# Kernel tuning notes

Hardware: AMD Instinct MI355X
Metric: run time of the kernel (lower is better)

Reference implementation:

```python
import jax, jax.numpy as jnp
import numpy as np

B, S, H, N_IN, N_OUT = 8, 2048, 16, 128, 128


def setup_inputs() -> dict:
    key = jax.random.key(0)
    k1, k2 = jax.random.split(key)
    inputs = jax.random.normal(k1, (B, S, H, N_IN), dtype=jnp.float32)
    # stacked ParameterList: W[h] is the (n_out, n_in) block for head h
    W = jax.random.normal(k2, (H, N_OUT, N_IN), dtype=jnp.float32) * 0.02
    return {"inputs": inputs, "W": W}


def reference(inputs, W):
    # Block-diagonal projection: each head h gets its own (n_out, n_in) matrix.
    # Equivalent to the torch loop of per-head GEMVs, expressed as one einsum.
    # inputs: [b, s, h, i], W: [h, o, i] -> out: [b, s, h, o]
    return jnp.einsum("bshi,hoi->bsho", inputs, W)
```

## Files before the change

kernel.cpp:

```cpp
#include <hip/hip_runtime.h>
#include <hip/hip_bf16.h>

typedef __attribute__((ext_vector_type(4))) float  f4;
typedef __attribute__((ext_vector_type(8))) short  short8;
typedef __attribute__((ext_vector_type(4))) float  f32x4;

static constexpr int NHEAD = 16;
static constexpr int NIN   = 128;
static constexpr int NOUT  = 128;
static constexpr int NROWS = 8 * 2048;
static constexpr int RSTR  = NHEAD * NIN;
static constexpr int ROWS_PER_BLOCK = 128;
static constexpr int BLOCKS_X = NROWS / ROWS_PER_BLOCK;

static __device__ inline unsigned short f2bfu(float f) {
  union { __hip_bfloat16 h; unsigned short u; } v;
  v.h = __float2bfloat16(f);
  return v.u;
}

static __device__ inline short8 cvt8(f4 a, f4 b) {
  short8 r;
  r[0] = (short)f2bfu(a[0]); r[1] = (short)f2bfu(a[1]);
  r[2] = (short)f2bfu(a[2]); r[3] = (short)f2bfu(a[3]);
  r[4] = (short)f2bfu(b[0]); r[5] = (short)f2bfu(b[1]);
  r[6] = (short)f2bfu(b[2]); r[7] = (short)f2bfu(b[3]);
  return r;
}

__global__ __launch_bounds__(512)
void bdp_kernel(const float* __restrict__ X, const float* __restrict__ W,
                float* __restrict__ O) {
  __shared__ short8 wtile[32][64];

  const int head = blockIdx.y;
  const int tid  = (int)threadIdx.x;
  const int lane = tid & 63;
  const int wid  = tid >> 6;
  const int lr   = lane & 15;
  const int lq   = lane >> 4;

  const int row0 = (int)blockIdx.x * ROWS_PER_BLOCK + wid * 16;
  const float* xr = X + (size_t)(row0 + lr) * RSTR + head * NIN;

  f4 xa[4], xb[4];
  #pragma unroll
  for (int kk = 0; kk < 4; ++kk) {
    const int koff = kk * 32 + lq * 8;
    xa[kk] = *reinterpret_cast<const f4*>(xr + koff);
    xb[kk] = *reinterpret_cast<const f4*>(xr + koff + 4);
  }

  const float* Wh = W + (size_t)head * NOUT * NIN;
  #pragma unroll
  for (int it = 0; it < 4; ++it) {
    const int frag = wid * 4 + it;
    const int n  = frag >> 2;
    const int kk = frag & 3;
    const float* src = Wh + (n * 16 + lr) * NIN + kk * 32 + lq * 8;
    f4 a = *reinterpret_cast<const f4*>(src);
    f4 b = *reinterpret_cast<const f4*>(src + 4);
    wtile[frag][lane] = cvt8(a, b);
  }
  __syncthreads();

  short8 xv[4];
  #pragma unroll
  for (int kk = 0; kk < 4; ++kk) xv[kk] = cvt8(xa[kk], xb[kk]);

  f32x4 acc[8];
  #pragma unroll
  for (int n = 0; n < 8; ++n) acc[n] = (f32x4){0.f, 0.f, 0.f, 0.f};

  #pragma unroll
  for (int kk = 0; kk < 4; ++kk) {
    #pragma unroll
    for (int n = 0; n < 8; ++n) {
      acc[n] = __builtin_amdgcn_mfma_f32_16x16x32_bf16(
          wtile[n * 4 + kk][lane], xv[kk], acc[n], 0, 0, 0);
    }
  }

  float* dst = O + (size_t)(row0 + lr) * RSTR + head * NOUT;
  #pragma unroll
  for (int n = 0; n < 8; ++n) {
    __builtin_nontemporal_store(acc[n], reinterpret_cast<f4*>(dst + n * 16 + lq * 4));
  }
}

extern "C" void kernel_launch(void* const* d_in, const int* in_sizes, int n_in,
                              void* d_out, int out_size, void* d_ws, size_t ws_size,
                              hipStream_t stream) {
  const float* X = (const float*)d_in[0];
  const float* W = (const float*)d_in[1];
  float* O = (float*)d_out;
  dim3 grid(BLOCKS_X, NHEAD);
  bdp_kernel<<<grid, dim3(512), 0, stream>>>(X, W, O);
}
```

Baseline: 61.00 us.

## Process four row tiles per block with double-buffered X prefetch

Each block now handles four 128-row tiles, so each staged W tile is reused across four tiles, and the grid shrinks by a factor of four. The next tile's X values are prefetched into registers two tiles ahead while the current tile's MFMAs run. Stores change from nontemporal to regular, and launch bounds request four waves per SIMD. The trade-offs are fewer blocks to spread across CUs and higher register pressure from the double-buffered X.

```diff
diff --git a/kernel.cpp b/kernel.cpp
--- a/kernel.cpp
+++ b/kernel.cpp
@@ -10,7 +10,8 @@
 static constexpr int NOUT  = 128;
 static constexpr int NROWS = 8 * 2048;
 static constexpr int RSTR  = NHEAD * NIN;
-static constexpr int ROWS_PER_BLOCK = 128;
+static constexpr int TILES = 4;
+static constexpr int ROWS_PER_BLOCK = 128 * TILES;
 static constexpr int BLOCKS_X = NROWS / ROWS_PER_BLOCK;
 
 static __device__ inline unsigned short f2bfu(float f) {
@@ -28,7 +29,7 @@
   return r;
 }
 
-__global__ __launch_bounds__(512)
+__global__ __launch_bounds__(512, 4)
 void bdp_kernel(const float* __restrict__ X, const float* __restrict__ W,
                 float* __restrict__ O) {
   __shared__ short8 wtile[32][64];
@@ -40,15 +41,24 @@
   const int lr   = lane & 15;
   const int lq   = lane >> 4;
 
-  const int row0 = (int)blockIdx.x * ROWS_PER_BLOCK + wid * 16;
-  const float* xr = X + (size_t)(row0 + lr) * RSTR + head * NIN;
+  const int rowbase = (int)blockIdx.x * ROWS_PER_BLOCK + wid * 16;
+  const float* xr = X + (size_t)(rowbase + lr) * RSTR + head * NIN;
 
-  f4 xa[4], xb[4];
+  f4 xs[2][8];
   #pragma unroll
   for (int kk = 0; kk < 4; ++kk) {
     const int koff = kk * 32 + lq * 8;
-    xa[kk] = *reinterpret_cast<const f4*>(xr + koff);
-    xb[kk] = *reinterpret_cast<const f4*>(xr + koff + 4);
+    xs[0][2*kk]   = *reinterpret_cast<const f4*>(xr + koff);
+    xs[0][2*kk+1] = *reinterpret_cast<const f4*>(xr + koff + 4);
+  }
+  {
+    const float* xr1 = xr + (size_t)128 * RSTR;
+    #pragma unroll
+    for (int kk = 0; kk < 4; ++kk) {
+      const int koff = kk * 32 + lq * 8;
+      xs[1][2*kk]   = *reinterpret_cast<const f4*>(xr1 + koff);
+      xs[1][2*kk+1] = *reinterpret_cast<const f4*>(xr1 + koff + 4);
+    }
   }
 
   const float* Wh = W + (size_t)head * NOUT * NIN;
@@ -64,27 +74,43 @@
   }
   __syncthreads();
 
-  short8 xv[4];
   #pragma unroll
-  for (int kk = 0; kk < 4; ++kk) xv[kk] = cvt8(xa[kk], xb[kk]);
+  for (int t = 0; t < TILES; ++t) {
+    const int slot = t & 1;
 
-  f32x4 acc[8];
-  #pragma unroll
-  for (int n = 0; n < 8; ++n) acc[n] = (f32x4){0.f, 0.f, 0.f, 0.f};
+    short8 xv[4];
+    #pragma unroll
+    for (int kk = 0; kk < 4; ++kk)
+      xv[kk] = cvt8(xs[slot][2*kk], xs[slot][2*kk+1]);
 
-  #pragma unroll
-  for (int kk = 0; kk < 4; ++kk) {
+    if (t + 2 < TILES) {
+      const float* xrn = xr + (size_t)(t + 2) * 128 * RSTR;
+      #pragma unroll
+      for (int kk = 0; kk < 4; ++kk) {
+        const int koff = kk * 32 + lq * 8;
+        xs[slot][2*kk]   = *reinterpret_cast<const f4*>(xrn + koff);
+        xs[slot][2*kk+1] = *reinterpret_cast<const f4*>(xrn + koff + 4);
+      }
+    }
+
+    f32x4 acc[8];
+    #pragma unroll
+    for (int n = 0; n < 8; ++n) acc[n] = (f32x4){0.f, 0.f, 0.f, 0.f};
+
+    #pragma unroll
+    for (int kk = 0; kk < 4; ++kk) {
+      #pragma unroll
+      for (int n = 0; n < 8; ++n) {
+        acc[n] = __builtin_amdgcn_mfma_f32_16x16x32_bf16(
+            wtile[n * 4 + kk][lane], xv[kk], acc[n], 0, 0, 0);
+      }
+    }
+
+    float* dst = O + (size_t)(rowbase + t * 128 + lr) * RSTR + head * NOUT;
     #pragma unroll
     for (int n = 0; n < 8; ++n) {
-      acc[n] = __builtin_amdgcn_mfma_f32_16x16x32_bf16(
-          wtile[n * 4 + kk][lane], xv[kk], acc[n], 0, 0, 0);
+      *reinterpret_cast<f4*>(dst + n * 16 + lq * 4) = acc[n];
     }
-  }
-
-  float* dst = O + (size_t)(row0 + lr) * RSTR + head * NOUT;
-  #pragma unroll
-  for (int n = 0; n < 8; ++n) {
-    __builtin_nontemporal_store(acc[n], reinterpret_cast<f4*>(dst + n * 16 + lq * 4));
   }
 }
 
```

After: 67.50 us. 1.11x slower.

## Process four row tiles per block with double-buffered input prefetch

Applied to the files above, without the earlier changes.

Each block now handles four 128-row tiles instead of one. The converted W tile in shared memory is reused across those tiles, and the next tile's inputs are prefetched into a second register set while the current tile's MFMAs run. The launch-bounds occupancy hint is raised, and output stores switch from nontemporal to regular stores. The grid shrinks by a factor of four, which lowers parallelism on a many-CU GPU and raises register pressure.

```diff
diff --git a/kernel.cpp b/kernel.cpp
--- a/kernel.cpp
+++ b/kernel.cpp
@@ -10,7 +10,8 @@
 static constexpr int NOUT  = 128;
 static constexpr int NROWS = 8 * 2048;
 static constexpr int RSTR  = NHEAD * NIN;
-static constexpr int ROWS_PER_BLOCK = 128;
+static constexpr int TILES = 4;
+static constexpr int ROWS_PER_BLOCK = 128 * TILES;
 static constexpr int BLOCKS_X = NROWS / ROWS_PER_BLOCK;
 
 static __device__ inline unsigned short f2bfu(float f) {
@@ -28,7 +29,7 @@
   return r;
 }
 
-__global__ __launch_bounds__(512)
+__global__ __launch_bounds__(512, 4)
 void bdp_kernel(const float* __restrict__ X, const float* __restrict__ W,
                 float* __restrict__ O) {
   __shared__ short8 wtile[32][64];
@@ -40,16 +41,26 @@
   const int lr   = lane & 15;
   const int lq   = lane >> 4;
 
-  const int row0 = (int)blockIdx.x * ROWS_PER_BLOCK + wid * 16;
-  const float* xr = X + (size_t)(row0 + lr) * RSTR + head * NIN;
+  const int rowbase = (int)blockIdx.x * ROWS_PER_BLOCK + wid * 16;
+  const float* xr = X + (size_t)(rowbase + lr) * RSTR + head * NIN;
 
-  f4 xa[4], xb[4];
+  f4 xs0[8], xs1[8];
   #pragma unroll
   for (int kk = 0; kk < 4; ++kk) {
     const int koff = kk * 32 + lq * 8;
-    xa[kk] = *reinterpret_cast<const f4*>(xr + koff);
-    xb[kk] = *reinterpret_cast<const f4*>(xr + koff + 4);
+    xs0[2*kk]   = *reinterpret_cast<const f4*>(xr + koff);
+    xs0[2*kk+1] = *reinterpret_cast<const f4*>(xr + koff + 4);
   }
+  {
+    const float* xr1 = xr + (size_t)128 * RSTR;
+    #pragma unroll
+    for (int kk = 0; kk < 4; ++kk) {
+      const int koff = kk * 32 + lq * 8;
+      xs1[2*kk]   = *reinterpret_cast<const f4*>(xr1 + koff);
+      xs1[2*kk+1] = *reinterpret_cast<const f4*>(xr1 + koff + 4);
+    }
+  }
+  __builtin_amdgcn_sched_barrier(0);
 
   const float* Wh = W + (size_t)head * NOUT * NIN;
   #pragma unroll
@@ -64,28 +75,40 @@
   }
   __syncthreads();
 
-  short8 xv[4];
-  #pragma unroll
-  for (int kk = 0; kk < 4; ++kk) xv[kk] = cvt8(xa[kk], xb[kk]);
-
-  f32x4 acc[8];
-  #pragma unroll
-  for (int n = 0; n < 8; ++n) acc[n] = (f32x4){0.f, 0.f, 0.f, 0.f};
-
-  #pragma unroll
-  for (int kk = 0; kk < 4; ++kk) {
-    #pragma unroll
-    for (int n = 0; n < 8; ++n) {
-      acc[n] = __builtin_amdgcn_mfma_f32_16x16x32_bf16(
-          wtile[n * 4 + kk][lane], xv[kk], acc[n], 0, 0, 0);
-    }
+#define TILE_BODY(xsC, T, PF)                                              \
+  {                                                                        \
+    f32x4 acc[8];                                                          \
+    _Pragma("unroll")                                                      \
+    for (int n = 0; n < 8; ++n) acc[n] = (f32x4){0.f, 0.f, 0.f, 0.f};      \
+    _Pragma("unroll")                                                      \
+    for (int kk = 0; kk < 4; ++kk) {                                       \
+      short8 xv = cvt8(xsC[2*kk], xsC[2*kk+1]);                            \
+      _Pragma("unroll")                                                    \
+      for (int n = 0; n < 8; ++n)                                          \
+        acc[n] = __builtin_amdgcn_mfma_f32_16x16x32_bf16(                  \
+            wtile[n*4+kk][lane], xv, acc[n], 0, 0, 0);                     \
+    }                                                                      \
+    if (PF) {                                                              \
+      const float* xrn = xr + (size_t)((T) + 2) * 128 * RSTR;              \
+      _Pragma("unroll")                                                    \
+      for (int kk = 0; kk < 4; ++kk) {                                     \
+        const int koff = kk * 32 + lq * 8;                                 \
+        xsC[2*kk]   = *reinterpret_cast<const f4*>(xrn + koff);            \
+        xsC[2*kk+1] = *reinterpret_cast<const f4*>(xrn + koff + 4);        \
+      }                                                                    \
+      __builtin_amdgcn_sched_barrier(0);                                   \
+    }                                                                      \
+    float* dst = O + (size_t)(rowbase + (T) * 128 + lr) * RSTR + head*NOUT;\
+    _Pragma("unroll")                                                      \
+    for (int n = 0; n < 8; ++n)                                            \
+      *reinterpret_cast<f4*>(dst + n * 16 + lq * 4) = acc[n];              \
   }
 
-  float* dst = O + (size_t)(row0 + lr) * RSTR + head * NOUT;
-  #pragma unroll
-  for (int n = 0; n < 8; ++n) {
-    __builtin_nontemporal_store(acc[n], reinterpret_cast<f4*>(dst + n * 16 + lq * 4));
-  }
+  TILE_BODY(xs0, 0, 1)
+  TILE_BODY(xs1, 1, 1)
+  TILE_BODY(xs0, 2, 0)
+  TILE_BODY(xs1, 3, 0)
+#undef TILE_BODY
 }
 
 extern "C" void kernel_launch(void* const* d_in, const int* in_sizes, int n_in,
```

After: 52.27 us. -14.3%, faster.

## Double-buffer X tiles via global_load_lds and loop over row tiles per block

Applied to the files above, without the earlier changes.

Each block now processes 512 rows in 16 tiles of 32 rows. It stages the input tiles asynchronously into swizzled, double-buffered LDS with global_load_lds, so loading the next tile overlaps the MFMA work on the current one. The converted weight tile is reused across more rows, and waves are split into two row groups by four output-column pairs. This adds a block-wide sync per tile, increases LDS use, and switches from nontemporal to normal stores. The kernel is memory-bound, so grid parallelism drops (512 blocks instead of 2048), which may hurt bandwidth saturation.

```diff
diff --git a/kernel.cpp b/kernel.cpp
--- a/kernel.cpp
+++ b/kernel.cpp
@@ -10,8 +10,13 @@
 static constexpr int NOUT  = 128;
 static constexpr int NROWS = 8 * 2048;
 static constexpr int RSTR  = NHEAD * NIN;
-static constexpr int ROWS_PER_BLOCK = 128;
+static constexpr int ROWS_PER_TILE  = 32;
+static constexpr int TILES          = 16;
+static constexpr int ROWS_PER_BLOCK = ROWS_PER_TILE * TILES;
 static constexpr int BLOCKS_X = NROWS / ROWS_PER_BLOCK;
+
+typedef __attribute__((address_space(3))) void  lds_void;
+typedef const __attribute__((address_space(1))) void g_void;
 
 static __device__ inline unsigned short f2bfu(float f) {
   union { __hip_bfloat16 h; unsigned short u; } v;
@@ -28,10 +33,11 @@
   return r;
 }
 
-__global__ __launch_bounds__(512)
+__global__ __launch_bounds__(512, 4)
 void bdp_kernel(const float* __restrict__ X, const float* __restrict__ W,
                 float* __restrict__ O) {
   __shared__ short8 wtile[32][64];
+  __shared__ f4 xbuf[2][1024];
 
   const int head = blockIdx.y;
   const int tid  = (int)threadIdx.x;
@@ -39,17 +45,30 @@
   const int wid  = tid >> 6;
   const int lr   = lane & 15;
   const int lq   = lane >> 4;
+  const int rg   = wid & 1;
+  const int nh   = wid >> 1;
 
-  const int row0 = (int)blockIdx.x * ROWS_PER_BLOCK + wid * 16;
-  const float* xr = X + (size_t)(row0 + lr) * RSTR + head * NIN;
+  const int rowblock0 = (int)blockIdx.x * ROWS_PER_BLOCK;
+  const char* Xh = (const char*)X + (size_t)head * NIN * 4;
 
-  f4 xa[4], xb[4];
-  #pragma unroll
-  for (int kk = 0; kk < 4; ++kk) {
-    const int koff = kk * 32 + lq * 8;
-    xa[kk] = *reinterpret_cast<const f4*>(xr + koff);
-    xb[kk] = *reinterpret_cast<const f4*>(xr + koff + 4);
+#define STAGE(bi, t)                                                       \
+  {                                                                        \
+    const size_t rb = (size_t)(rowblock0 + (t) * ROWS_PER_TILE);           \
+    _Pragma("unroll")                                                      \
+    for (int r = 0; r < 2; ++r) {                                          \
+      const int off = tid * 16 + r * 8192;         \
+      const int row = off >> 9;                                            \
+      const int wb  = off & 511;                                           \
+      const int wbs = wb ^ ((row & 7) << 4);                               \
+      const char* g = Xh + (rb + row) * (size_t)(RSTR * 4) + wbs;          \
+      __builtin_amdgcn_global_load_lds(                                    \
+          (g_void*)g,                                                      \
+          (lds_void*)((char*)&xbuf[bi][0] + r * 8192 + wid * 1024),        \
+          16, 0, 0);                                                       \
+    }                                                                      \
   }
+
+  STAGE(0, 0)
 
   const float* Wh = W + (size_t)head * NOUT * NIN;
   #pragma unroll
@@ -64,28 +83,34 @@
   }
   __syncthreads();
 
-  short8 xv[4];
-  #pragma unroll
-  for (int kk = 0; kk < 4; ++kk) xv[kk] = cvt8(xa[kk], xb[kk]);
+  for (int t = 0; t < TILES; ++t) {
+    const int bi = t & 1;
+    if (t + 1 < TILES) STAGE(bi ^ 1, t + 1)
 
-  f32x4 acc[8];
-  #pragma unroll
-  for (int n = 0; n < 8; ++n) acc[n] = (f32x4){0.f, 0.f, 0.f, 0.f};
+    const char* xb = (const char*)&xbuf[bi][0];
+    const int sw = (lr & 7) << 4;
+    f32x4 acc0 = (f32x4){0.f, 0.f, 0.f, 0.f};
+    f32x4 acc1 = (f32x4){0.f, 0.f, 0.f, 0.f};
+    #pragma unroll
+    for (int kk = 0; kk < 4; ++kk) {
+      const int u0 = (rg * 16 + lr) * 512 + kk * 128 + lq * 32;
+      f4 a = *reinterpret_cast<const f4*>(xb + (u0 ^ sw));
+      f4 b = *reinterpret_cast<const f4*>(xb + ((u0 + 16) ^ sw));
+      short8 xv = cvt8(a, b);
+      acc0 = __builtin_amdgcn_mfma_f32_16x16x32_bf16(
+          wtile[(nh * 2 + 0) * 4 + kk][lane], xv, acc0, 0, 0, 0);
+      acc1 = __builtin_amdgcn_mfma_f32_16x16x32_bf16(
+          wtile[(nh * 2 + 1) * 4 + kk][lane], xv, acc1, 0, 0, 0);
+    }
 
-  #pragma unroll
-  for (int kk = 0; kk < 4; ++kk) {
-    #pragma unroll
-    for (int n = 0; n < 8; ++n) {
-      acc[n] = __builtin_amdgcn_mfma_f32_16x16x32_bf16(
-          wtile[n * 4 + kk][lane], xv[kk], acc[n], 0, 0, 0);
-    }
+    float* dst = O + (size_t)(rowblock0 + t * ROWS_PER_TILE + rg * 16 + lr) * RSTR
+               + head * NOUT;
+    *reinterpret_cast<f4*>(dst + (nh * 2 + 0) * 16 + lq * 4) = acc0;
+    *reinterpret_cast<f4*>(dst + (nh * 2 + 1) * 16 + lq * 4) = acc1;
+
+    __syncthreads();
   }
-
-  float* dst = O + (size_t)(row0 + lr) * RSTR + head * NOUT;
-  #pragma unroll
-  for (int n = 0; n < 8; ++n) {
-    __builtin_nontemporal_store(acc[n], reinterpret_cast<f4*>(dst + n * 16 + lq * 4));
-  }
+#undef STAGE
 }
 
 extern "C" void kernel_launch(void* const* d_in, const int* in_sizes, int n_in,
```

Measured after the change: 59.03 us. 3.2% less time.
